# Optimization experiments

Hardware: AMD Instinct MI355X
Metric: run time of the kernel (lower is better)

Reference implementation:

```python
import jax, jax.numpy as jnp
import numpy as np

B = 2048          # batch_size_large + batch_size_small
H = 4096          # hidden dim (hardcoded in module)
R = 64            # r_large (padded rank)
NA = 64           # num_adapters_small + num_adapters_large


def setup_inputs() -> dict:
    key = jax.random.key(0)
    kx, kw, ka = jax.random.split(key, 3)
    x = jax.random.normal(kx, (B, 1, H), dtype=jnp.float16)
    wids = jax.random.randint(kw, (B,), 0, NA, dtype=jnp.int32)
    lora_A = (jax.random.normal(ka, (NA, H, R), dtype=jnp.float16) * 0.02).astype(jnp.float16)
    return {"x": x, "wids": wids, "lora_A": lora_A}


def reference(x, wids, lora_A):
    # Per-sample adapter gather + batched matmul (bgmv):
    # out[b] = x[b] @ lora_A[wids[b]]  -> [B, 1, R]
    w = jnp.take(lora_A, wids, axis=0)           # [B, H, R]
    return jnp.einsum("bsh,bhr->bsr", x, w)      # [B, 1, R]
```

## Files before the change

kernel.cpp:

```cpp
#include <hip/hip_runtime.h>
#include <stdint.h>

#define B_TOT 2048
#define H_DIM 4096
#define R_DIM 64
#define NA_DIM 64
#define NS 32
#define KS (H_DIM / NS)
#define LW 68
#define X_ELEMS (B_TOT*H_DIM)
#define W_ELEMS (B_TOT)
#define A_ELEMS (NA_DIM*H_DIM*R_DIM)

typedef _Float16 f16x8 __attribute__((ext_vector_type(8)));
typedef float    f32x4 __attribute__((ext_vector_type(4)));

__device__ __forceinline__ uint32_t pkf16(float a, float b) {
  auto h = __builtin_amdgcn_cvt_pkrtz(a, b);
  union { decltype(h) v; uint32_t u; } cv; cv.v = h; return cv.u;
}

__global__ __launch_bounds__(256, 4)
void k_lora_mfma4(const float* __restrict__ x, const int* __restrict__ wids,
                  const float* __restrict__ A, uint16_t* __restrict__ part) {
  __shared__ __align__(16) uint32_t X_lds[16 * LW];
  __shared__ uint16_t sbin[B_TOT];
  __shared__ int sn;

  const int bx = blockIdx.x;
  const int a = bx & 63, ks = bx >> 6;
  const int t = threadIdx.x;
  const int w = t >> 6, l = t & 63;
  const int ml = l & 15;
  const int kg = l >> 4;

  const float* Abase = A + ((size_t)a * H_DIM + (size_t)ks * KS) * R_DIM
                         + (size_t)(w * 16 + ml);
  f16x8 afr[4];
#pragma unroll
  for (int kst = 0; kst < 4; ++kst) {
    const float* p = Abase + (size_t)(kst * 32 + kg * 8) * R_DIM;
    float v0 = p[0],   v1 = p[64],  v2 = p[128], v3 = p[192];
    float v4 = p[256], v5 = p[320], v6 = p[384], v7 = p[448];
    union { uint4 u; f16x8 h; } cv;
    cv.u.x = pkf16(v0, v1); cv.u.y = pkf16(v2, v3);
    cv.u.z = pkf16(v4, v5); cv.u.w = pkf16(v6, v7);
    afr[kst] = cv.h;
  }

  if (w == 0) {
    int v[32];
#pragma unroll
    for (int i = 0; i < 32; ++i) v[i] = wids[i * 64 + l];
    int cnt = 0;
#pragma unroll
    for (int i = 0; i < 32; ++i) {
      bool hit = (v[i] == a);
      unsigned long long m = __ballot(hit);
      if (hit) sbin[cnt + __popcll(m & ((1ull << l) - 1ull))] = (uint16_t)(i * 64 + l);
      cnt += __popcll(m);
    }
    if (l == 0) sn = cnt;
  }
  __syncthreads();
  const int n = sn;
  if (n == 0) return;

  const int m_st = t >> 4, q_st = t & 15;

  for (int mg = 0; mg * 16 < n; ++mg) {
    const int base = mg * 16;
    {
      int sidx = base + m_st; if (sidx > n - 1) sidx = n - 1;
      const float* xr = x + (size_t)sbin[sidx] * H_DIM + (size_t)ks * KS;
      const int k = q_st * 8;
      float4 u0 = *(const float4*)(xr + k);
      float4 u1 = *(const float4*)(xr + k + 4);
      uint4 pw;
      pw.x = pkf16(u0.x, u0.y); pw.y = pkf16(u0.z, u0.w);
      pw.z = pkf16(u1.x, u1.y); pw.w = pkf16(u1.z, u1.w);
      *(uint4*)&X_lds[m_st * LW + q_st * 4] = pw;
    }
    __syncthreads();

    f32x4 acc = {0.f, 0.f, 0.f, 0.f};
#pragma unroll
    for (int kst = 0; kst < 4; ++kst) {
      f16x8 xf = *(const f16x8*)(X_lds + ml * LW + kst * 16 + kg * 4);
      acc = __builtin_amdgcn_mfma_f32_16x16x32_f16(xf, afr[kst], acc, 0, 0, 0);
    }

#pragma unroll
    for (int i = 0; i < 4; ++i) {
      const int sidx = base + kg * 4 + i;
      if (sidx < n) {
        union { _Float16 h; uint16_t u; } cv; cv.h = (_Float16)acc[i];
        part[(size_t)ks * (B_TOT * R_DIM) +
             (size_t)sbin[sidx] * R_DIM + w * 16 + ml] = cv.u;
      }
    }
    if ((mg + 1) * 16 < n) __syncthreads();
  }
}

__global__ __launch_bounds__(256)
void k_reduce32h(const uint16_t* __restrict__ part, float* __restrict__ out) {
  const int t = blockIdx.x * 256 + threadIdx.x;
  const int b = t >> 4, r4 = t & 15;
  const size_t o = (size_t)b * R_DIM + r4 * 4;
  float v0 = 0.f, v1 = 0.f, v2 = 0.f, v3 = 0.f;
#pragma unroll
  for (int p = 0; p < NS; ++p) {
    uint2 q = *(const uint2*)&part[(size_t)p * (B_TOT * R_DIM) + o];
    union { uint32_t u; _Float16 h[2]; } c0, c1;
    c0.u = q.x; c1.u = q.y;
    v0 += (float)c0.h[0]; v1 += (float)c0.h[1];
    v2 += (float)c1.h[0]; v3 += (float)c1.h[1];
  }
  *(float4*)&out[o] = make_float4(v0, v1, v2, v3);
}

__global__ __launch_bounds__(256)
void k_naive_f32(const float* __restrict__ x, const int* __restrict__ wids,
                 const float* __restrict__ A, float* __restrict__ out) {
  __shared__ float red[256];
  const int b = blockIdx.x;
  const int t = threadIdx.x;
  const int r = t & 63;
  const int q = t >> 6;
  const int a = wids[b];
  const float* xrow = x + (size_t)b * H_DIM;
  const float* Aad  = A + (size_t)a * H_DIM * R_DIM + r;
  float acc = 0.f;
  const int h0 = q * (H_DIM / 4), h1 = h0 + (H_DIM / 4);
  for (int h = h0; h < h1; ++h) acc += xrow[h] * Aad[(size_t)h * R_DIM];
  red[t] = acc;
  __syncthreads();
  if (t < 64) {
    out[(size_t)b * R_DIM + t] = red[t] + red[t + 64] + red[t + 128] + red[t + 192];
  }
}

extern "C" void kernel_launch(void* const* d_in, const int* in_sizes, int n_in,
                              void* d_out, int out_size, void* d_ws, size_t ws_size,
                              hipStream_t stream) {
  const void* px = nullptr; const void* pw = nullptr; const void* pa = nullptr;
  for (int i = 0; i < n_in; ++i) {
    if (in_sizes[i] == X_ELEMS) px = d_in[i];
    else if (in_sizes[i] == W_ELEMS) pw = d_in[i];
    else if (in_sizes[i] == A_ELEMS) pa = d_in[i];
  }
  if (!px || !pw || !pa) { px = d_in[0]; pw = d_in[1]; pa = d_in[2]; }

  const float* x    = (const float*)px;
  const int*   wids = (const int*)pw;
  const float* A    = (const float*)pa;
  float* out = (float*)d_out;
  (void)out_size;

  const size_t need = (size_t)NS * B_TOT * R_DIM * sizeof(uint16_t);
  if (ws_size >= need) {
    uint16_t* part = (uint16_t*)d_ws;
    k_lora_mfma4<<<dim3(NA_DIM * NS), dim3(256), 0, stream>>>(x, wids, A, part);
    k_reduce32h<<<dim3(128), dim3(256), 0, stream>>>(part, out);
  } else {
    k_naive_f32<<<dim3(B_TOT), dim3(256), 0, stream>>>(x, wids, A, out);
  }
}
```

Measured before the change: 27.07 us.

## Move adapter binning to separate kernel and double-buffer X tile in LDS

```diff
diff --git a/kernel.cpp b/kernel.cpp
--- a/kernel.cpp
+++ b/kernel.cpp
@@ -20,12 +20,31 @@
   union { decltype(h) v; uint32_t u; } cv; cv.v = h; return cv.u;
 }
 
+__global__ __launch_bounds__(64)
+void k_bin64(const int* __restrict__ wids, int* __restrict__ cnt,
+             uint16_t* __restrict__ bin) {
+  const int a = blockIdx.x;
+  const int l = threadIdx.x;
+  int v[32];
+#pragma unroll
+  for (int i = 0; i < 32; ++i) v[i] = wids[i * 64 + l];
+  int c = 0;
+#pragma unroll
+  for (int i = 0; i < 32; ++i) {
+    bool hit = (v[i] == a);
+    unsigned long long m = __ballot(hit);
+    if (hit) bin[a * B_TOT + c + __popcll(m & ((1ull << l) - 1ull))] =
+        (uint16_t)(i * 64 + l);
+    c += __popcll(m);
+  }
+  if (l == 0) cnt[a] = c;
+}
+
 __global__ __launch_bounds__(256, 4)
-void k_lora_mfma4(const float* __restrict__ x, const int* __restrict__ wids,
-                  const float* __restrict__ A, uint16_t* __restrict__ part) {
-  __shared__ __align__(16) uint32_t X_lds[16 * LW];
-  __shared__ uint16_t sbin[B_TOT];
-  __shared__ int sn;
+void k_lora_mfma5(const float* __restrict__ x, const int* __restrict__ cnt,
+                  const uint16_t* __restrict__ bin, const float* __restrict__ A,
+                  uint16_t* __restrict__ part) {
+  __shared__ __align__(16) uint32_t X_lds[2 * 16 * LW];
 
   const int bx = blockIdx.x;
   const int a = bx & 63, ks = bx >> 6;
@@ -33,6 +52,12 @@
   const int w = t >> 6, l = t & 63;
   const int ml = l & 15;
   const int kg = l >> 4;
+
+  const int n = cnt[a];
+  if (n == 0) return;
+  const uint16_t* mybin = bin + a * B_TOT;
+
+  const int m_st = t >> 4, q_st = t & 15;
 
   const float* Abase = A + ((size_t)a * H_DIM + (size_t)ks * KS) * R_DIM
                          + (size_t)(w * 16 + ml);
@@ -48,45 +73,26 @@
     afr[kst] = cv.h;
   }
 
-  if (w == 0) {
-    int v[32];
-#pragma unroll
-    for (int i = 0; i < 32; ++i) v[i] = wids[i * 64 + l];
-    int cnt = 0;
-#pragma unroll
-    for (int i = 0; i < 32; ++i) {
-      bool hit = (v[i] == a);
-      unsigned long long m = __ballot(hit);
-      if (hit) sbin[cnt + __popcll(m & ((1ull << l) - 1ull))] = (uint16_t)(i * 64 + l);
-      cnt += __popcll(m);
-    }
-    if (l == 0) sn = cnt;
-  }
-  __syncthreads();
-  const int n = sn;
-  if (n == 0) return;
-
-  const int m_st = t >> 4, q_st = t & 15;
-
   for (int mg = 0; mg * 16 < n; ++mg) {
     const int base = mg * 16;
+    const int buf = (mg & 1) * (16 * LW);
     {
       int sidx = base + m_st; if (sidx > n - 1) sidx = n - 1;
-      const float* xr = x + (size_t)sbin[sidx] * H_DIM + (size_t)ks * KS;
+      const float* xr = x + (size_t)mybin[sidx] * H_DIM + (size_t)ks * KS;
       const int k = q_st * 8;
       float4 u0 = *(const float4*)(xr + k);
       float4 u1 = *(const float4*)(xr + k + 4);
       uint4 pw;
       pw.x = pkf16(u0.x, u0.y); pw.y = pkf16(u0.z, u0.w);
       pw.z = pkf16(u1.x, u1.y); pw.w = pkf16(u1.z, u1.w);
-      *(uint4*)&X_lds[m_st * LW + q_st * 4] = pw;
+      *(uint4*)&X_lds[buf + m_st * LW + q_st * 4] = pw;
     }
     __syncthreads();
 
     f32x4 acc = {0.f, 0.f, 0.f, 0.f};
 #pragma unroll
     for (int kst = 0; kst < 4; ++kst) {
-      f16x8 xf = *(const f16x8*)(X_lds + ml * LW + kst * 16 + kg * 4);
+      f16x8 xf = *(const f16x8*)(X_lds + buf + ml * LW + kst * 16 + kg * 4);
       acc = __builtin_amdgcn_mfma_f32_16x16x32_f16(xf, afr[kst], acc, 0, 0, 0);
     }
 
@@ -96,10 +102,9 @@
       if (sidx < n) {
         union { _Float16 h; uint16_t u; } cv; cv.h = (_Float16)acc[i];
         part[(size_t)ks * (B_TOT * R_DIM) +
-             (size_t)sbin[sidx] * R_DIM + w * 16 + ml] = cv.u;
+             (size_t)mybin[sidx] * R_DIM + w * 16 + ml] = cv.u;
       }
     }
-    if ((mg + 1) * 16 < n) __syncthreads();
   }
 }
 
@@ -158,10 +163,14 @@
   float* out = (float*)d_out;
   (void)out_size;
 
-  const size_t need = (size_t)NS * B_TOT * R_DIM * sizeof(uint16_t);
+  const size_t need = 1024 + 512 * 1024 +
+                      (size_t)NS * B_TOT * R_DIM * sizeof(uint16_t);
   if (ws_size >= need) {
-    uint16_t* part = (uint16_t*)d_ws;
-    k_lora_mfma4<<<dim3(NA_DIM * NS), dim3(256), 0, stream>>>(x, wids, A, part);
+    int*      cnt  = (int*)d_ws;
+    uint16_t* bin  = (uint16_t*)((char*)d_ws + 1024);
+    uint16_t* part = (uint16_t*)((char*)d_ws + 1024 + 512 * 1024);
+    k_bin64<<<dim3(NA_DIM), dim3(64), 0, stream>>>(wids, cnt, bin);
+    k_lora_mfma5<<<dim3(NA_DIM * NS), dim3(256), 0, stream>>>(x, cnt, bin, A, part);
     k_reduce32h<<<dim3(128), dim3(256), 0, stream>>>(part, out);
   } else {
     k_naive_f32<<<dim3(B_TOT), dim3(256), 0, stream>>>(x, wids, A, out);
```

Result: slower. 32.92 us (+21.6%).
